# Kernel tuning notes

Measured on AMD Instinct MI355X. Metric: run time of the kernel, lower is better.

## Reference

```python
import jax, jax.numpy as jnp
import numpy as np

BATCH, LATENT_DIM, NUM_QUBITS = 32768, 2048, 24


def setup_inputs() -> dict:
    key = jax.random.key(0)
    k1, k2, k3, k4 = jax.random.split(key, 4)
    return {
        "latent": jax.random.normal(k1, (BATCH, LATENT_DIM), dtype=jnp.float32),
        "W": jax.random.normal(k2, (NUM_QUBITS, LATENT_DIM), dtype=jnp.float32) * (1.0 / np.sqrt(LATENT_DIM)),
        "b": jax.random.normal(k3, (NUM_QUBITS,), dtype=jnp.float32) * 0.01,
        "params": jax.random.normal(k4, (NUM_QUBITS, 3), dtype=jnp.float32),
    }


def reference(latent, W, b, params):
    # Classical projection: (B, L) @ (L, Q) + (Q,) -> per-qubit encoding angle a
    a = jnp.einsum("bl,ql->bq", latent, W) + b  # (B, Q)
    # Circuit per qubit: RY(a) on |0>, then Rot(phi, theta, omega) = RZ(omega)RY(theta)RZ(phi).
    # Bloch vector after RY(a): (sin a, 0, cos a). RZ(phi) then RY(theta) give
    # z = cos(a)cos(theta) - sin(a)cos(phi)sin(theta); final RZ(omega) leaves <Z> unchanged.
    phi = params[:, 0]    # (Q,)
    theta = params[:, 1]  # (Q,)
    return jnp.cos(a) * jnp.cos(theta) - jnp.sin(a) * (jnp.cos(phi) * jnp.sin(theta))
```

## Files before the change

### kernel.cpp

```cpp
#include <hip/hip_runtime.h>
#include <cstdint>


#define NQ 24
#define LDIM 2048
#define BATCH 32768
#define NKT 64

typedef __attribute__((ext_vector_type(8))) short bf16x8;
typedef __attribute__((ext_vector_type(4))) float f32x4;

union U4 { uint4 u; bf16x8 s; };

__device__ __forceinline__ uint cvt_pk_bf16(float lo, float hi) {
    uint r;
    asm("v_cvt_pk_bf16_f32 %0, %1, %2" : "=v"(r) : "v"(lo), "v"(hi));
    return r;
}

struct Grp { float4 a0[4]; float4 a1[4]; uint4 b0[4]; uint4 b1[4]; };

__device__ __forceinline__ void issueG(Grp& g, const float* ap, const uint4* bp, int t0) {
    #pragma unroll
    for (int i = 0; i < 4; i++) {
        g.a0[i] = *(const float4*)(ap + (t0 + i) * 32);
        g.a1[i] = *(const float4*)(ap + (t0 + i) * 32 + 4);
    }
    #pragma unroll
    for (int i = 0; i < 4; i++) {
        g.b0[i] = bp[(t0 + i) * 128];
        g.b1[i] = bp[(t0 + i) * 128 + 64];
    }
}

__device__ __forceinline__ void computeT(const float4 a0, const float4 a1,
                                         const uint4 b0u, const uint4 b1u,
                                         f32x4& c0, f32x4& c1) {
    uint h0 = cvt_pk_bf16(a0.x, a0.y);
    uint h1 = cvt_pk_bf16(a0.z, a0.w);
    uint h2 = cvt_pk_bf16(a1.x, a1.y);
    uint h3 = cvt_pk_bf16(a1.z, a1.w);
    float r0 = __uint_as_float(h0 << 16), r1 = __uint_as_float(h0 & 0xFFFF0000u);
    float r2 = __uint_as_float(h1 << 16), r3 = __uint_as_float(h1 & 0xFFFF0000u);
    float r4 = __uint_as_float(h2 << 16), r5 = __uint_as_float(h2 & 0xFFFF0000u);
    float r6 = __uint_as_float(h3 << 16), r7 = __uint_as_float(h3 & 0xFFFF0000u);
    uint l0 = cvt_pk_bf16(a0.x - r0, a0.y - r1);
    uint l1 = cvt_pk_bf16(a0.z - r2, a0.w - r3);
    uint l2 = cvt_pk_bf16(a1.x - r4, a1.y - r5);
    uint l3 = cvt_pk_bf16(a1.z - r6, a1.w - r7);
    U4 ah, al, b0, b1;
    ah.u = make_uint4(h0, h1, h2, h3);
    al.u = make_uint4(l0, l1, l2, l3);
    b0.u = b0u;
    b1.u = b1u;
    c0 = __builtin_amdgcn_mfma_f32_16x16x32_bf16(ah.s, b0.s, c0, 0, 0, 0);
    c1 = __builtin_amdgcn_mfma_f32_16x16x32_bf16(ah.s, b1.s, c1, 0, 0, 0);
    c0 = __builtin_amdgcn_mfma_f32_16x16x32_bf16(al.s, b0.s, c0, 0, 0, 0);
    c1 = __builtin_amdgcn_mfma_f32_16x16x32_bf16(al.s, b1.s, c1, 0, 0, 0);
}

__device__ __forceinline__ void computeG(const Grp& g, f32x4& c0, f32x4& c1) {
    #pragma unroll
    for (int i = 0; i < 4; i++)
        computeT(g.a0[i], g.a1[i], g.b0[i], g.b1[i], c0, c1);
}

__global__ __launch_bounds__(256, 2) void qll_main(
    const float* __restrict__ latent,
    const uint4* __restrict__ wb,
    const float* __restrict__ bvec,
    const float* __restrict__ ctv,
    const float* __restrict__ csv,
    float* __restrict__ out)
{
    const int tid  = threadIdx.x;
    const int wave = tid >> 6;
    const int lane = tid & 63;
    const int mrow = lane & 15;
    const int kgrp = lane >> 4;
    const int row0 = (blockIdx.x * 4 + wave) * 16;

    const float* ap = latent + (size_t)(row0 + mrow) * LDIM + kgrp * 8;
    const uint4* bp = wb + lane;

    f32x4 c0 = {0.f, 0.f, 0.f, 0.f};
    f32x4 c1 = {0.f, 0.f, 0.f, 0.f};

    Grp GA, GB;
    issueG(GA, ap, bp, 0);
    issueG(GB, ap, bp, 4);

    #pragma unroll 1
    for (int t = 0; t <= NKT - 16; t += 8) {
        computeG(GA, c0, c1); issueG(GA, ap, bp, t + 8);
        computeG(GB, c0, c1); issueG(GB, ap, bp, t + 12);
    }
    computeG(GA, c0, c1);
    computeG(GB, c0, c1);

    #pragma unroll
    for (int qt = 0; qt < 2; qt++) {
        const int q = qt * 16 + mrow;
        const bool valid = (q < NQ);
        const float bv = valid ? bvec[q] : 0.f;
        const float ct = valid ? ctv[q]  : 0.f;
        const float cs = valid ? csv[q]  : 0.f;
        const f32x4 c = qt ? c1 : c0;
        #pragma unroll
        for (int r = 0; r < 4; r++) {
            const int row = row0 + kgrp * 4 + r;
            const float a = c[r] + bv;
            float s, co;
            __sincosf(a, &s, &co);
            if (valid) out[(size_t)row * NQ + q] = co * ct - s * cs;
        }
    }
}

__global__ __launch_bounds__(256) void qll_prep(
    const float* __restrict__ W, const float* __restrict__ params,
    ushort* __restrict__ wb, float* __restrict__ ctcs)
{
    const int idx = blockIdx.x * 256 + threadIdx.x;
    const int kt  = idx >> 10;
    const int rem = idx & 1023;
    const int qt  = rem >> 9;
    const int l   = (rem >> 3) & 63;
    const int e   = rem & 7;
    const int q   = qt * 16 + (l & 15);
    const int k   = kt * 32 + (l >> 4) * 8 + e;
    float v = (q < NQ) ? W[q * LDIM + k] : 0.f;
    uint u = __float_as_uint(v);
    wb[idx] = (ushort)((u + 0x7FFF + ((u >> 16) & 1)) >> 16);
    if (idx < NQ) {
        float phi = params[3 * idx + 0];
        float th  = params[3 * idx + 1];
        ctcs[idx]      = cosf(th);
        ctcs[NQ + idx] = cosf(phi) * sinf(th);
    }
}

extern "C" void kernel_launch(void* const* d_in, const int* in_sizes, int n_in,
                              void* d_out, int out_size, void* d_ws, size_t ws_size,
                              hipStream_t stream) {
    (void)in_sizes; (void)n_in; (void)out_size; (void)ws_size;
    const float* latent = (const float*)d_in[0];
    const float* W      = (const float*)d_in[1];
    const float* bvec   = (const float*)d_in[2];
    const float* params = (const float*)d_in[3];
    float* out  = (float*)d_out;
    ushort* wb  = (ushort*)d_ws;
    float* ctcs = (float*)d_ws + 32768;

    hipLaunchKernelGGL(qll_prep, dim3(256), dim3(256), 0, stream,
                       W, params, wb, ctcs);
    hipLaunchKernelGGL(qll_main, dim3(BATCH / 64), dim3(256), 0, stream,
                       latent, (const uint4*)wb, bvec, ctcs, ctcs + NQ, out);
}
```

Before: 57.28 us.

## Stage latent panels into LDS via direct global-to-LDS loads with double buffering

Replaces the per-lane register loads of latent rows with global_load_lds DMA into a per-wave double-buffered LDS panel, using an XOR swizzle so rows are fetched as fully coalesced 512-byte segments and later read back from LDS without bank conflicts. The goal is better global access coalescing than the old strided per-lane float4 reads, and lower register pressure. In exchange it adds 64KB of LDS per block, which may limit occupancy to one or two blocks per CU. It also relies on manual vmcnt waits with no LDS barrier, because each wave only reads its own buffer.

```diff
diff --git a/kernel.cpp b/kernel.cpp
--- a/kernel.cpp
+++ b/kernel.cpp
@@ -5,12 +5,21 @@
 #define NQ 24
 #define LDIM 2048
 #define BATCH 32768
-#define NKT 64
+#define NPANEL 16
 
 typedef __attribute__((ext_vector_type(8))) short bf16x8;
 typedef __attribute__((ext_vector_type(4))) float f32x4;
 
 union U4 { uint4 u; bf16x8 s; };
+
+typedef const __attribute__((address_space(1))) void* gas_t;
+typedef __attribute__((address_space(3))) void* las_t;
+
+__device__ __forceinline__ void gload_lds16(const float* g, float* l) {
+    __builtin_amdgcn_global_load_lds((gas_t)g, (las_t)l, 16, 0, 0);
+}
+
+#define CVMCNT(n) asm volatile("s_waitcnt vmcnt(" #n ")" ::: "memory")
 
 __device__ __forceinline__ uint cvt_pk_bf16(float lo, float hi) {
     uint r;
@@ -18,18 +27,25 @@
     return r;
 }
 
-struct Grp { float4 a0[4]; float4 a1[4]; uint4 b0[4]; uint4 b1[4]; };
+struct BGrp { uint4 b0[4]; uint4 b1[4]; };
 
-__device__ __forceinline__ void issueG(Grp& g, const float* ap, const uint4* bp, int t0) {
+__device__ __forceinline__ void loadB(BGrp& g, const uint4* bp, int p) {
     #pragma unroll
-    for (int i = 0; i < 4; i++) {
-        g.a0[i] = *(const float4*)(ap + (t0 + i) * 32);
-        g.a1[i] = *(const float4*)(ap + (t0 + i) * 32 + 4);
+    for (int t = 0; t < 4; t++) {
+        g.b0[t] = bp[(p * 4 + t) * 128];
+        g.b1[t] = bp[(p * 4 + t) * 128 + 64];
     }
+}
+
+__device__ __forceinline__ void stagePanel(const float* lsrc, float* ldst,
+                                           int p, int lane) {
+    const int half = lane >> 5;
+    const int l32  = lane & 31;
     #pragma unroll
-    for (int i = 0; i < 4; i++) {
-        g.b0[i] = bp[(t0 + i) * 128];
-        g.b1[i] = bp[(t0 + i) * 128 + 64];
+    for (int i = 0; i < 8; i++) {
+        const int r = 2 * i + half;
+        const int s = l32 ^ (r & 7);
+        gload_lds16(lsrc + (size_t)r * LDIM + p * 128 + s * 4, ldst + i * 256);
     }
 }
 
@@ -59,10 +75,18 @@
     c1 = __builtin_amdgcn_mfma_f32_16x16x32_bf16(al.s, b1.s, c1, 0, 0, 0);
 }
 
-__device__ __forceinline__ void computeG(const Grp& g, f32x4& c0, f32x4& c1) {
+__device__ __forceinline__ void computePanel(const float* __restrict__ lbuf,
+                                             const BGrp& g, int mrow, int kgrp,
+                                             f32x4& c0, f32x4& c1) {
+    const int base = mrow * 128;
+    const int e0 = (((kgrp << 1) ^ (mrow & 7)) << 2);
+    const int e1 = ((((kgrp << 1) | 1) ^ (mrow & 7)) << 2);
     #pragma unroll
-    for (int i = 0; i < 4; i++)
-        computeT(g.a0[i], g.a1[i], g.b0[i], g.b1[i], c0, c1);
+    for (int t = 0; t < 4; t++) {
+        float4 a0 = *(const float4*)(lbuf + base + t * 32 + e0);
+        float4 a1 = *(const float4*)(lbuf + base + t * 32 + e1);
+        computeT(a0, a1, g.b0[t], g.b1[t], c0, c1);
+    }
 }
 
 __global__ __launch_bounds__(256, 2) void qll_main(
@@ -73,6 +97,8 @@
     const float* __restrict__ csv,
     float* __restrict__ out)
 {
+    __shared__ __align__(16) float lds[4][2][2048];
+
     const int tid  = threadIdx.x;
     const int wave = tid >> 6;
     const int lane = tid & 63;
@@ -80,23 +106,37 @@
     const int kgrp = lane >> 4;
     const int row0 = (blockIdx.x * 4 + wave) * 16;
 
-    const float* ap = latent + (size_t)(row0 + mrow) * LDIM + kgrp * 8;
-    const uint4* bp = wb + lane;
+    const float* lsrc = latent + (size_t)row0 * LDIM;
+    const uint4* bp   = wb + lane;
+
+    float* lbuf0 = &lds[wave][0][0];
+    float* lbuf1 = &lds[wave][1][0];
 
     f32x4 c0 = {0.f, 0.f, 0.f, 0.f};
     f32x4 c1 = {0.f, 0.f, 0.f, 0.f};
 
-    Grp GA, GB;
-    issueG(GA, ap, bp, 0);
-    issueG(GB, ap, bp, 4);
+    BGrp B0, B1;
+    stagePanel(lsrc, lbuf0, 0, lane);
+    loadB(B0, bp, 0);
 
     #pragma unroll 1
-    for (int t = 0; t <= NKT - 16; t += 8) {
-        computeG(GA, c0, c1); issueG(GA, ap, bp, t + 8);
-        computeG(GB, c0, c1); issueG(GB, ap, bp, t + 12);
+    for (int i = 0; i < 7; i++) {
+        const int p = 2 * i;
+        stagePanel(lsrc, lbuf1, p + 1, lane);
+        loadB(B1, bp, p + 1);
+        CVMCNT(16);
+        computePanel(lbuf0, B0, mrow, kgrp, c0, c1);
+        stagePanel(lsrc, lbuf0, p + 2, lane);
+        loadB(B0, bp, p + 2);
+        CVMCNT(16);
+        computePanel(lbuf1, B1, mrow, kgrp, c0, c1);
     }
-    computeG(GA, c0, c1);
-    computeG(GB, c0, c1);
+    stagePanel(lsrc, lbuf1, 15, lane);
+    loadB(B1, bp, 15);
+    CVMCNT(16);
+    computePanel(lbuf0, B0, mrow, kgrp, c0, c1);
+    CVMCNT(0);
+    computePanel(lbuf1, B1, mrow, kgrp, c0, c1);
 
     #pragma unroll
     for (int qt = 0; qt < 2; qt++) {
```

After: 50.73 us. 11.4% less time.
